# Optimization experiments

Hardware: AMD Instinct MI355X
Metric: run time of the kernel (lower is better)

The kernel has to match this reference:

```python
import jax, jax.numpy as jnp
import numpy as np

N = 100000
E = 1600000
NFEAT = 128
NHID = 16
HEADS = 4
NCLASS = 40
NEG_SLOPE = 0.2
BN_EPS = 1e-5


def setup_inputs() -> dict:
    key = jax.random.key(0)
    ks = jax.random.split(key, 16)
    HC = NHID * HEADS  # 64
    x = jax.random.normal(ks[0], (N, NFEAT), dtype=jnp.float32)
    edge_index = jax.random.randint(ks[1], (2, E), 0, N, dtype=jnp.int64)
    def glorot(k, shape, fan_in):
        return jax.random.normal(k, shape, dtype=jnp.float32) * (1.0 / np.sqrt(fan_in))
    return {
        "x": x,
        "edge_index": edge_index,
        # layer 1: GATConv(NFEAT -> NHID, heads=HEADS, concat=True)
        "W1": glorot(ks[2], (NFEAT, HC), NFEAT),
        "att_src1": glorot(ks[3], (HEADS, NHID), NHID),
        "att_dst1": glorot(ks[4], (HEADS, NHID), NHID),
        "bias1": jnp.zeros((HC,), dtype=jnp.float32),
        # BatchNorm1d(HC), eval mode (running stats)
        "bn_gamma": jnp.ones((HC,), dtype=jnp.float32),
        "bn_beta": jnp.zeros((HC,), dtype=jnp.float32),
        "bn_mean": jax.random.normal(ks[5], (HC,), dtype=jnp.float32) * 0.1,
        "bn_var": jax.random.uniform(ks[6], (HC,), dtype=jnp.float32, minval=0.5, maxval=1.5),
        # layer 2: GATConv(HC -> NCLASS, heads=1, concat=False)
        "W2": glorot(ks[7], (HC, NCLASS), HC),
        "att_src2": glorot(ks[8], (1, NCLASS), NCLASS),
        "att_dst2": glorot(ks[9], (1, NCLASS), NCLASS),
        "bias2": jnp.zeros((NCLASS,), dtype=jnp.float32),
    }


def gat_conv(x, src, dst, W, att_src, att_dst, bias, concat):
    """PyG GATConv (eval; self-loops assumed already appended to src/dst)."""
    H, C = att_src.shape
    n = x.shape[0]
    h = (x @ W).reshape(n, H, C)                         # [N,H,C]
    a_s = (h * att_src[None]).sum(-1)                    # [N,H]
    a_d = (h * att_dst[None]).sum(-1)                    # [N,H]
    alpha = jax.nn.leaky_relu(a_s[src] + a_d[dst], NEG_SLOPE)  # [Et,H]
    # segment softmax over incoming edges of each destination node
    amax = jax.ops.segment_max(alpha, dst, num_segments=n)    # [N,H]
    ex = jnp.exp(alpha - amax[dst])
    denom = jax.ops.segment_sum(ex, dst, num_segments=n)
    coef = ex / denom[dst]                               # [Et,H]
    msg = h[src] * coef[:, :, None]                      # [Et,H,C]
    out = jax.ops.segment_sum(msg, dst, num_segments=n)  # [N,H,C]
    out = out.reshape(n, H * C) if concat else out.mean(axis=1)
    return out + bias


def reference(x, edge_index, W1, att_src1, att_dst1, bias1,
              bn_gamma, bn_beta, bn_mean, bn_var,
              W2, att_src2, att_dst2, bias2):
    n = x.shape[0]
    loops = jnp.arange(n, dtype=edge_index.dtype)
    src = jnp.concatenate([edge_index[0], loops])
    dst = jnp.concatenate([edge_index[1], loops])
    h = gat_conv(x, src, dst, W1, att_src1, att_dst1, bias1, concat=True)
    h = (h - bn_mean) * jax.lax.rsqrt(bn_var + BN_EPS) * bn_gamma + bn_beta
    h = jax.nn.relu(h)  # dropout is identity in eval
    out = gat_conv(h, src, dst, W2, att_src2, att_dst2, bias2, concat=False)
    return out
```

## Files before the change

kernel.cpp:

```cpp
#include <hip/hip_runtime.h>
#include <hip/hip_bf16.h>
#include <hip/hip_fp16.h>

#define NFEAT  128
#define HC     64
#define HEADS  4
#define NHID   16
#define NCLASS 40
#define NEG    0.2f
#define BN_EPS 1e-5f

#define BK_SH   9
#define CHUNK   8192
#define STAGE   12288

typedef _Float16 half8_t __attribute__((ext_vector_type(8)));
typedef float    f32x4_t __attribute__((ext_vector_type(4)));

__device__ __forceinline__ float leaky(float a) { return (a > 0.f) ? a : NEG * a; }

__global__ __launch_bounds__(256) void k_gemm1(
    const float* __restrict__ x, const float* __restrict__ W1,
    const float* __restrict__ att_s, const float* __restrict__ att_d,
    __half* __restrict__ h1, float* __restrict__ as1, float* __restrict__ ad1,
    int n)
{
    const int wave = threadIdx.x >> 6, lane = threadIdx.x & 63;
    const int quad = lane >> 4, l16 = lane & 15;

    half8_t bfrag[4][4];
    #pragma unroll
    for (int ks = 0; ks < 4; ++ks)
        #pragma unroll
        for (int ct = 0; ct < 4; ++ct)
            #pragma unroll
            for (int j = 0; j < 8; ++j)
                bfrag[ks][ct][j] =
                    (_Float16)W1[(ks * 32 + quad * 8 + j) * HC + ct * 16 + l16];

    float avs[4], avd[4];
    #pragma unroll
    for (int ct = 0; ct < 4; ++ct) {
        avs[ct] = att_s[ct * 16 + l16];
        avd[ct] = att_d[ct * 16 + l16];
    }

    const int nslab = (n + 15) >> 4;
    for (int slab = blockIdx.x * 4 + wave; slab < nslab; slab += gridDim.x * 4) {
        const int rowbase = slab * 16;
        const int arow = min(rowbase + l16, n - 1);
        const float* xp = x + (size_t)arow * NFEAT;

        f32x4_t acc[4] = {{0.f,0.f,0.f,0.f},{0.f,0.f,0.f,0.f},
                          {0.f,0.f,0.f,0.f},{0.f,0.f,0.f,0.f}};
        #pragma unroll
        for (int ks = 0; ks < 4; ++ks) {
            const float4 xa = *(const float4*)(xp + ks * 32 + quad * 8);
            const float4 xb = *(const float4*)(xp + ks * 32 + quad * 8 + 4);
            half8_t af;
            af[0] = (_Float16)xa.x; af[1] = (_Float16)xa.y;
            af[2] = (_Float16)xa.z; af[3] = (_Float16)xa.w;
            af[4] = (_Float16)xb.x; af[5] = (_Float16)xb.y;
            af[6] = (_Float16)xb.z; af[7] = (_Float16)xb.w;
            #pragma unroll
            for (int ct = 0; ct < 4; ++ct)
                acc[ct] = __builtin_amdgcn_mfma_f32_16x16x32_f16(
                    af, bfrag[ks][ct], acc[ct], 0, 0, 0);
        }

        #pragma unroll
        for (int reg = 0; reg < 4; ++reg) {
            const int row = rowbase + quad * 4 + reg;
            const bool valid = row < n;

            float4 ps, pd;
            ps.x = acc[0][reg] * avs[0]; pd.x = acc[0][reg] * avd[0];
            ps.y = acc[1][reg] * avs[1]; pd.y = acc[1][reg] * avd[1];
            ps.z = acc[2][reg] * avs[2]; pd.z = acc[2][reg] * avd[2];
            ps.w = acc[3][reg] * avs[3]; pd.w = acc[3][reg] * avd[3];
            #pragma unroll
            for (int off = 8; off >= 1; off >>= 1) {
                ps.x += __shfl_xor(ps.x, off, 64); pd.x += __shfl_xor(pd.x, off, 64);
                ps.y += __shfl_xor(ps.y, off, 64); pd.y += __shfl_xor(pd.y, off, 64);
                ps.z += __shfl_xor(ps.z, off, 64); pd.z += __shfl_xor(pd.z, off, 64);
                ps.w += __shfl_xor(ps.w, off, 64); pd.w += __shfl_xor(pd.w, off, 64);
            }
            if (valid) {
                #pragma unroll
                for (int ct = 0; ct < 4; ++ct)
                    h1[(size_t)row * HC + ct * 16 + l16] =
                        __float2half_rn(acc[ct][reg]);
                if (l16 == 0) {
                    *(float4*)(as1 + (size_t)row * HEADS) = ps;
                    *(float4*)(ad1 + (size_t)row * HEADS) = pd;
                }
            }
        }
    }
}

__global__ __launch_bounds__(256) void k_hist(
    const int* __restrict__ edst, int* __restrict__ hist, int E, int nbk)
{
    __shared__ int lh[256];
    const int w = blockIdx.x, t = threadIdx.x;
    for (int i = t; i < nbk; i += 256) lh[i] = 0;
    __syncthreads();
    const int lo = w * CHUNK, hi = min(E, lo + CHUNK);
    for (int e = lo + t; e < hi; e += 256)
        atomicAdd(&lh[edst[e] >> BK_SH], 1);
    __syncthreads();
    for (int i = t; i < nbk; i += 256) hist[(size_t)w * nbk + i] = lh[i];
}

__global__ __launch_bounds__(256) void k_colscan(
    int* __restrict__ hist, int* __restrict__ colsum, int nbk, int nw)
{
    __shared__ int wred[4];
    const int b = blockIdx.x, t = threadIdx.x;
    const int lane = t & 63, w = t >> 6;
    const int v = (t < nw) ? hist[(size_t)t * nbk + b] : 0;
    int sc = v;
    #pragma unroll
    for (int off = 1; off < 64; off <<= 1) {
        int u = __shfl_up(sc, off, 64);
        if (lane >= off) sc += u;
    }
    if (lane == 63) wred[w] = sc;
    __syncthreads();
    if (t == 0) { int a = 0; for (int i = 0; i < 4; ++i) { int xx = wred[i]; wred[i] = a; a += xx; } }
    __syncthreads();
    const int excl = sc - v + wred[w];
    if (t < nw) hist[(size_t)t * nbk + b] = excl;
    if (t == nw - 1) colsum[b] = excl + v;
}

__global__ __launch_bounds__(256) void k_bscan(
    const int* __restrict__ colsum, int* __restrict__ bstart, int nbk, int E)
{
    __shared__ int wred[4];
    const int t = threadIdx.x, lane = t & 63, w = t >> 6;
    const int v = (t < nbk) ? colsum[t] : 0;
    int sc = v;
    #pragma unroll
    for (int off = 1; off < 64; off <<= 1) {
        int u = __shfl_up(sc, off, 64);
        if (lane >= off) sc += u;
    }
    if (lane == 63) wred[w] = sc;
    __syncthreads();
    if (t == 0) { int a = 0; for (int i = 0; i < 4; ++i) { int xx = wred[i]; wred[i] = a; a += xx; } }
    __syncthreads();
    if (t < nbk) bstart[t] = sc - v + wred[w];
    if (t == 0) bstart[nbk] = E;
}

__global__ __launch_bounds__(256) void k_scatter(
    const int* __restrict__ esrc, const int* __restrict__ edst,
    const int* __restrict__ hist, const int* __restrict__ bstart,
    int2* __restrict__ pairs, int E, int nbk)
{
    __shared__ int cur[256];
    const int w = blockIdx.x, t = threadIdx.x;
    for (int i = t; i < nbk; i += 256)
        cur[i] = bstart[i] + hist[(size_t)w * nbk + i];
    __syncthreads();
    const int lo = w * CHUNK, hi = min(E, lo + CHUNK);
    for (int e = lo + t; e < hi; e += 256) {
        const int s = esrc[e], d = edst[e];
        const int pos = atomicAdd(&cur[d >> BK_SH], 1);
        pairs[pos] = make_int2(s, d);
    }
}

__global__ __launch_bounds__(256) void k_build(
    const int2* __restrict__ pairs, const int* __restrict__ bstart,
    int* __restrict__ rowptr, int* __restrict__ csr, int n, int nbk)
{
    __shared__ int cnt[512];
    __shared__ int cur[512];
    __shared__ int stage[STAGE];
    __shared__ int wred[4];
    const int b = blockIdx.x, t = threadIdx.x;
    const int base = bstart[b], eend = bstart[b + 1], m = eend - base;
    const int n0 = b << BK_SH;
    const int nn = min(512, n - n0);

    cnt[t] = 0; cnt[t + 256] = 0;
    __syncthreads();
    for (int e = base + t; e < eend; e += 256)
        atomicAdd(&cnt[pairs[e].y - n0], 1);
    __syncthreads();

    const int c0 = cnt[2 * t], c1 = cnt[2 * t + 1];
    const int s = c0 + c1;
    const int lane = t & 63, w = t >> 6;
    int sc = s;
    #pragma unroll
    for (int off = 1; off < 64; off <<= 1) {
        int u = __shfl_up(sc, off, 64);
        if (lane >= off) sc += u;
    }
    if (lane == 63) wred[w] = sc;
    __syncthreads();
    if (t == 0) { int a = 0; for (int i = 0; i < 4; ++i) { int xx = wred[i]; wred[i] = a; a += xx; } }
    __syncthreads();
    const int excl = sc - s + wred[w];
    cur[2 * t]     = excl;
    cur[2 * t + 1] = excl + c0;
    if (2 * t < nn)     rowptr[n0 + 2 * t]     = base + excl + c0;
    if (2 * t + 1 < nn) rowptr[n0 + 2 * t + 1] = base + excl + c0 + c1;
    __syncthreads();

    for (int e = base + t; e < eend; e += 256) {
        const int2 p = pairs[e];
        const int loc = atomicAdd(&cur[p.y - n0], 1);
        if (loc < STAGE) stage[loc] = p.x;
        else             csr[base + loc] = p.x;
    }
    __syncthreads();
    const int lim = min(m, STAGE);
    for (int i = t; i < lim; i += 256) csr[base + i] = stage[i];
}

__global__ __launch_bounds__(256) void k_agg1(
    const int* __restrict__ csr, const int* __restrict__ rowptr,
    const __half* __restrict__ h1, const float* __restrict__ as1,
    const float* __restrict__ ad1,
    const float* __restrict__ bias1, const float* __restrict__ gamma,
    const float* __restrict__ beta, const float* __restrict__ mean,
    const float* __restrict__ var,
    const float* __restrict__ W2, const float* __restrict__ ats2,
    const float* __restrict__ atd2,
    __half* __restrict__ g, float* __restrict__ as2o, float* __restrict__ ad2o,
    int n)
{
    __shared__ float sW[NCLASS * HC];
    __shared__ float sh[16][68];
    __shared__ float sE[16][132];
    __shared__ int   sS[16][33];
    for (int i = threadIdx.x; i < NCLASS * HC; i += 256) sW[i] = W2[i];
    __syncthreads();

    const int gi = threadIdx.x >> 4;
    const int q  = threadIdx.x & 15;
    const int myh = q >> 2;

    const float4 b1v = *(const float4*)(bias1 + 4 * q);
    const float4 gmv = *(const float4*)(gamma + 4 * q);
    const float4 vrv = *(const float4*)(var   + 4 * q);
    const float4 mnv = *(const float4*)(mean  + 4 * q);
    const float4 btv = *(const float4*)(beta  + 4 * q);
    float4 scv, shv;
    scv.x = gmv.x * rsqrtf(vrv.x + BN_EPS);
    scv.y = gmv.y * rsqrtf(vrv.y + BN_EPS);
    scv.z = gmv.z * rsqrtf(vrv.z + BN_EPS);
    scv.w = gmv.w * rsqrtf(vrv.w + BN_EPS);
    shv.x = btv.x - mnv.x * scv.x;
    shv.y = btv.y - mnv.y * scv.y;
    shv.z = btv.z - mnv.z * scv.z;
    shv.w = btv.w - mnv.w * scv.w;
    float4 at2 = {0.f, 0.f, 0.f, 0.f}, dt2 = {0.f, 0.f, 0.f, 0.f};
    if (q < 10) {
        at2 = *(const float4*)(ats2 + 4 * q);
        dt2 = *(const float4*)(atd2 + 4 * q);
    }

    for (int node0 = blockIdx.x * 16; node0 < n; node0 += gridDim.x * 16) {
        const int node = node0 + gi;
        if (node >= n) continue;

        const float4 adv = *(const float4*)(ad1 + node * HEADS);
        const float4 sv4 = *(const float4*)(as1 + node * HEADS);
        float4 eself;
        eself.x = __expf(leaky(sv4.x + adv.x));
        eself.y = __expf(leaky(sv4.y + adv.y));
        eself.z = __expf(leaky(sv4.z + adv.z));
        eself.w = __expf(leaky(sv4.w + adv.w));
        const float es = (myh == 0) ? eself.x : (myh == 1) ? eself.y
                       : (myh == 2) ? eself.z : eself.w;

        float2 raws = *(const float2*)(h1 + (size_t)node * HC + 4 * q);
        const float2 s0 = __half22float2(*(__half2*)&raws.x);
        const float2 s1 = __half22float2(*(__half2*)&raws.y);
        float4 acc;
        acc.x = es * s0.x; acc.y = es * s0.y;
        acc.z = es * s1.x; acc.w = es * s1.y;
        float4 dpart = {0.f, 0.f, 0.f, 0.f};

        const int start = (node == 0) ? 0 : rowptr[node - 1];
        const int end   = rowptr[node];

        for (int base = start; base < end; base += 32) {
            const int m = min(32, end - base);
            float4 ea = {0.f, 0.f, 0.f, 0.f}, eb = {0.f, 0.f, 0.f, 0.f};
            int ia = 0, ib = 0;
            if (q < m) {
                ia = csr[base + q];
                const float4 s4 = *(const float4*)(as1 + (size_t)ia * HEADS);
                ea.x = __expf(leaky(s4.x + adv.x));
                ea.y = __expf(leaky(s4.y + adv.y));
                ea.z = __expf(leaky(s4.z + adv.z));
                ea.w = __expf(leaky(s4.w + adv.w));
            }
            if (q + 16 < m) {
                ib = csr[base + q + 16];
                const float4 s4 = *(const float4*)(as1 + (size_t)ib * HEADS);
                eb.x = __expf(leaky(s4.x + adv.x));
                eb.y = __expf(leaky(s4.y + adv.y));
                eb.z = __expf(leaky(s4.z + adv.z));
                eb.w = __expf(leaky(s4.w + adv.w));
            }
            dpart.x += ea.x + eb.x; dpart.y += ea.y + eb.y;
            dpart.z += ea.z + eb.z; dpart.w += ea.w + eb.w;
            *(float4*)&sE[gi][4 * q] = ea;
            *(float4*)&sE[gi][4 * (q + 16)] = eb;
            sS[gi][q] = ia; sS[gi][q + 16] = ib;
            __threadfence_block();

            int j = 0;
            for (; j + 2 <= m; j += 2) {
                const int sa = sS[gi][j], sb = sS[gi][j + 1];
                const float fa = sE[gi][4 * j + myh];
                const float fb = sE[gi][4 * (j + 1) + myh];
                const float2 ra = *(const float2*)(h1 + (size_t)sa * HC + 4 * q);
                const float2 rb = *(const float2*)(h1 + (size_t)sb * HC + 4 * q);
                const float2 a0 = __half22float2(*(const __half2*)&ra.x);
                const float2 a1 = __half22float2(*(const __half2*)&ra.y);
                const float2 b0 = __half22float2(*(const __half2*)&rb.x);
                const float2 b1 = __half22float2(*(const __half2*)&rb.y);
                acc.x = fmaf(fa, a0.x, acc.x); acc.y = fmaf(fa, a0.y, acc.y);
                acc.z = fmaf(fa, a1.x, acc.z); acc.w = fmaf(fa, a1.y, acc.w);
                acc.x = fmaf(fb, b0.x, acc.x); acc.y = fmaf(fb, b0.y, acc.y);
                acc.z = fmaf(fb, b1.x, acc.z); acc.w = fmaf(fb, b1.y, acc.w);
            }
            if (j < m) {
                const int sa = sS[gi][j];
                const float fa = sE[gi][4 * j + myh];
                const float2 ra = *(const float2*)(h1 + (size_t)sa * HC + 4 * q);
                const float2 a0 = __half22float2(*(const __half2*)&ra.x);
                const float2 a1 = __half22float2(*(const __half2*)&ra.y);
                acc.x = fmaf(fa, a0.x, acc.x); acc.y = fmaf(fa, a0.y, acc.y);
                acc.z = fmaf(fa, a1.x, acc.z); acc.w = fmaf(fa, a1.y, acc.w);
            }
            __threadfence_block();
        }

        #pragma unroll
        for (int off = 8; off >= 1; off >>= 1) {
            dpart.x += __shfl_xor(dpart.x, off, 64);
            dpart.y += __shfl_xor(dpart.y, off, 64);
            dpart.z += __shfl_xor(dpart.z, off, 64);
            dpart.w += __shfl_xor(dpart.w, off, 64);
        }
        const float den = es + ((myh == 0) ? dpart.x : (myh == 1) ? dpart.y
                               : (myh == 2) ? dpart.z : dpart.w);
        const float rden = 1.f / den;

        float4 v;
        v.x = fmaxf(fmaf(acc.x * rden + b1v.x, scv.x, shv.x), 0.f);
        v.y = fmaxf(fmaf(acc.y * rden + b1v.y, scv.y, shv.y), 0.f);
        v.z = fmaxf(fmaf(acc.z * rden + b1v.z, scv.z, shv.z), 0.f);
        v.w = fmaxf(fmaf(acc.w * rden + b1v.w, scv.w, shv.w), 0.f);
        *(float4*)&sh[gi][4 * q] = v;
        __threadfence_block();

        float4 gacc = {0.f, 0.f, 0.f, 0.f};
        if (q < 10) {
            #pragma unroll 8
            for (int k = 0; k < HC; ++k) {
                const float hk = sh[gi][k];
                const float4 wv = *(const float4*)&sW[k * NCLASS + 4 * q];
                gacc.x = fmaf(hk, wv.x, gacc.x);
                gacc.y = fmaf(hk, wv.y, gacc.y);
                gacc.z = fmaf(hk, wv.z, gacc.z);
                gacc.w = fmaf(hk, wv.w, gacc.w);
            }
        }
        __half2 p0 = __float22half2_rn({gacc.x, gacc.y});
        __half2 p1 = __float22half2_rn({gacc.z, gacc.w});
        float2 packed; *(__half2*)&packed.x = p0; *(__half2*)&packed.y = p1;
        *(float2*)(g + (size_t)node * HC + 4 * q) = packed;

        float sv = gacc.x * at2.x + gacc.y * at2.y + gacc.z * at2.z + gacc.w * at2.w;
        float dv = gacc.x * dt2.x + gacc.y * dt2.y + gacc.z * dt2.z + gacc.w * dt2.w;
        #pragma unroll
        for (int off = 8; off >= 1; off >>= 1) {
            sv += __shfl_xor(sv, off, 64);
            dv += __shfl_xor(dv, off, 64);
        }
        if (q == 0) { as2o[node] = sv; ad2o[node] = dv; }
        __threadfence_block();
    }
}

__global__ __launch_bounds__(256) void k_agg2(
    const int* __restrict__ csr, const int* __restrict__ rowptr,
    const __half* __restrict__ g, const float* __restrict__ as2,
    const float* __restrict__ ad2, const float* __restrict__ bias2,
    float* __restrict__ out, int n)
{
    __shared__ float sE[16][34];
    __shared__ int   sS[16][33];
    const int gi = threadIdx.x >> 4;
    const int q  = threadIdx.x & 15;

    float4 b2v = {0.f, 0.f, 0.f, 0.f};
    if (q < 10) b2v = *(const float4*)(bias2 + 4 * q);

    for (int node0 = blockIdx.x * 16; node0 < n; node0 += gridDim.x * 16) {
        const int node = node0 + gi;
        if (node >= n) continue;

        const float ad2d = ad2[node];
        const float eself = __expf(leaky(as2[node] + ad2d));

        float2 raws = *(const float2*)(g + (size_t)node * HC + 4 * q);
        const float2 s0 = __half22float2(*(__half2*)&raws.x);
        const float2 s1 = __half22float2(*(__half2*)&raws.y);
        float4 acc;
        acc.x = eself * s0.x; acc.y = eself * s0.y;
        acc.z = eself * s1.x; acc.w = eself * s1.y;
        float dpart = 0.f;

        const int start = (node == 0) ? 0 : rowptr[node - 1];
        const int end   = rowptr[node];

        for (int base = start; base < end; base += 32) {
            const int m = min(32, end - base);
            float ea = 0.f, eb = 0.f;
            int ia = 0, ib = 0;
            if (q < m) {
                ia = csr[base + q];
                ea = __expf(leaky(as2[ia] + ad2d));
            }
            if (q + 16 < m) {
                ib = csr[base + q + 16];
                eb = __expf(leaky(as2[ib] + ad2d));
            }
            dpart += ea + eb;
            sE[gi][q] = ea; sE[gi][q + 16] = eb;
            sS[gi][q] = ia; sS[gi][q + 16] = ib;
            __threadfence_block();

            int j = 0;
            for (; j + 2 <= m; j += 2) {
                const int sa = sS[gi][j], sb = sS[gi][j + 1];
                const float fa = sE[gi][j], fb = sE[gi][j + 1];
                const float2 ra = *(const float2*)(g + (size_t)sa * HC + 4 * q);
                const float2 rb = *(const float2*)(g + (size_t)sb * HC + 4 * q);
                const float2 a0 = __half22float2(*(const __half2*)&ra.x);
                const float2 a1 = __half22float2(*(const __half2*)&ra.y);
                const float2 b0 = __half22float2(*(const __half2*)&rb.x);
                const float2 b1 = __half22float2(*(const __half2*)&rb.y);
                acc.x = fmaf(fa, a0.x, acc.x); acc.y = fmaf(fa, a0.y, acc.y);
                acc.z = fmaf(fa, a1.x, acc.z); acc.w = fmaf(fa, a1.y, acc.w);
                acc.x = fmaf(fb, b0.x, acc.x); acc.y = fmaf(fb, b0.y, acc.y);
                acc.z = fmaf(fb, b1.x, acc.z); acc.w = fmaf(fb, b1.y, acc.w);
            }
            if (j < m) {
                const int sa = sS[gi][j];
                const float fa = sE[gi][j];
                const float2 ra = *(const float2*)(g + (size_t)sa * HC + 4 * q);
                const float2 a0 = __half22float2(*(const __half2*)&ra.x);
                const float2 a1 = __half22float2(*(const __half2*)&ra.y);
                acc.x = fmaf(fa, a0.x, acc.x); acc.y = fmaf(fa, a0.y, acc.y);
                acc.z = fmaf(fa, a1.x, acc.z); acc.w = fmaf(fa, a1.y, acc.w);
            }
            __threadfence_block();
        }

        #pragma unroll
        for (int off = 8; off >= 1; off >>= 1)
            dpart += __shfl_xor(dpart, off, 64);
        const float rden = 1.f / (dpart + eself);

        if (q < 10) {
            float4 r;
            r.x = acc.x * rden + b2v.x;
            r.y = acc.y * rden + b2v.y;
            r.z = acc.z * rden + b2v.z;
            r.w = acc.w * rden + b2v.w;
            *(float4*)(out + (size_t)node * NCLASS + 4 * q) = r;
        }
    }
}

extern "C" void kernel_launch(void* const* d_in, const int* in_sizes, int n_in,
                              void* d_out, int out_size, void* d_ws, size_t ws_size,
                              hipStream_t stream)
{
    const float* x    = (const float*)d_in[0];
    const int*   ei   = (const int*)  d_in[1];
    const float* W1   = (const float*)d_in[2];
    const float* as1w = (const float*)d_in[3];
    const float* ad1w = (const float*)d_in[4];
    const float* b1   = (const float*)d_in[5];
    const float* gm   = (const float*)d_in[6];
    const float* bt   = (const float*)d_in[7];
    const float* mn   = (const float*)d_in[8];
    const float* vr   = (const float*)d_in[9];
    const float* W2   = (const float*)d_in[10];
    const float* as2w = (const float*)d_in[11];
    const float* ad2w = (const float*)d_in[12];
    const float* b2   = (const float*)d_in[13];

    const int n = in_sizes[0] / NFEAT;
    const int E = in_sizes[1] / 2;
    const int* esrc = ei;
    const int* edst = ei + E;

    const int nbk = (n + 511) >> BK_SH;
    const int nw  = (E + CHUNK - 1) / CHUNK;

    float*  ws   = (float*)d_ws;
    __half* h1   = (__half*)ws;
    float*  a_s1 = ws   + (size_t)n * 32;
    float*  a_d1 = a_s1 + (size_t)n * 4;
    __half* gbuf = (__half*)(a_d1 + (size_t)n * 4);
    float*  a_s2 = a_d1 + (size_t)n * 4 + (size_t)n * 32;
    float*  a_d2 = a_s2 + n;
    int2*   pairs  = (int2*)(a_d2 + n);
    int*    csr    = (int*)(pairs + E);
    int*    rowptr = csr + E;
    int*    hist   = rowptr + n;
    int*    colsum = hist + (size_t)nw * nbk;
    int*    bstart = colsum + nbk;
    float*  outv = (float*)d_out;

    const int nblk = (n + 15) / 16;

    k_hist   <<<nw, 256, 0, stream>>>(edst, hist, E, nbk);
    k_colscan<<<nbk, 256, 0, stream>>>(hist, colsum, nbk, nw);
    k_bscan  <<<1, 256, 0, stream>>>(colsum, bstart, nbk, E);
    k_scatter<<<nw, 256, 0, stream>>>(esrc, edst, hist, bstart, pairs, E, nbk);
    k_build  <<<nbk, 256, 0, stream>>>(pairs, bstart, rowptr, csr, n, nbk);
    k_gemm1  <<<512, 256, 0, stream>>>(x, W1, as1w, ad1w, h1, a_s1, a_d1, n);
    k_agg1   <<<nblk, 256, 0, stream>>>(csr, rowptr, h1, a_s1, a_d1, b1, gm, bt, mn, vr,
                                        W2, as2w, ad2w, gbuf, a_s2, a_d2, n);
    k_agg2   <<<nblk, 256, 0, stream>>>(csr, rowptr, gbuf, a_s2, a_d2, b2, outv, n);
}
```

Measured before the change: 295.4 us.

## Sort nodes by in-degree for balanced aggregation, prefetch gathers, fp16 W2 in LDS

Adds a degree histogram, a scan and a fill pass that build a permutation grouping nodes of similar in-degree. Both aggregation kernels then process nodes in that order, so the 16-thread groups within a wave have similar loop trip counts and less divergence. The neighbor gather loops are software-pipelined so the next pair of rows is loaded before the current pair is used. W2 is stored as fp16 in shared memory to halve its LDS footprint. The costs are three extra small kernels plus a memset, scattered node accesses through perm, and slightly lower precision in the second-layer projection.

Result: slower. 594.1 us (+101.1%).

```diff
diff --git a/kernel.cpp b/kernel.cpp
--- a/kernel.cpp
+++ b/kernel.cpp
@@ -15,6 +15,7 @@
 #define STAGE   12288
 
 typedef _Float16 half8_t __attribute__((ext_vector_type(8)));
+typedef _Float16 half4_t __attribute__((ext_vector_type(4)));
 typedef float    f32x4_t __attribute__((ext_vector_type(4)));
 
 __device__ __forceinline__ float leaky(float a) { return (a > 0.f) ? a : NEG * a; }
@@ -223,8 +224,52 @@
     for (int i = t; i < lim; i += 256) csr[base + i] = stage[i];
 }
 
+__global__ __launch_bounds__(256) void k_dhist(
+    const int* __restrict__ rowptr, int* __restrict__ dhist, int n)
+{
+    __shared__ int lh[128];
+    if (threadIdx.x < 128) lh[threadIdx.x] = 0;
+    __syncthreads();
+    for (int i = blockIdx.x * 256 + threadIdx.x; i < n; i += gridDim.x * 256) {
+        const int d = min(rowptr[i] - (i ? rowptr[i - 1] : 0), 127);
+        atomicAdd(&lh[d], 1);
+    }
+    __syncthreads();
+    if (threadIdx.x < 128 && lh[threadIdx.x])
+        atomicAdd(&dhist[threadIdx.x], lh[threadIdx.x]);
+}
+
+__global__ __launch_bounds__(128) void k_dscan(
+    const int* __restrict__ dhist, int* __restrict__ dcur)
+{
+    __shared__ int ws2[2];
+    const int t = threadIdx.x, lane = t & 63, w = t >> 6;
+    const int v = dhist[t];
+    int sc = v;
+    #pragma unroll
+    for (int off = 1; off < 64; off <<= 1) {
+        int u = __shfl_up(sc, off, 64);
+        if (lane >= off) sc += u;
+    }
+    if (lane == 63) ws2[w] = sc;
+    __syncthreads();
+    dcur[t] = sc - v + ((w == 1) ? ws2[0] : 0);
+}
+
+__global__ __launch_bounds__(256) void k_dfill(
+    const int* __restrict__ rowptr, int* __restrict__ dcur,
+    int* __restrict__ perm, int n)
+{
+    for (int i = blockIdx.x * 256 + threadIdx.x; i < n; i += gridDim.x * 256) {
+        const int d = min(rowptr[i] - (i ? rowptr[i - 1] : 0), 127);
+        const int pos = atomicAdd(&dcur[d], 1);
+        perm[pos] = i;
+    }
+}
+
 __global__ __launch_bounds__(256) void k_agg1(
     const int* __restrict__ csr, const int* __restrict__ rowptr,
+    const int* __restrict__ perm,
     const __half* __restrict__ h1, const float* __restrict__ as1,
     const float* __restrict__ ad1,
     const float* __restrict__ bias1, const float* __restrict__ gamma,
@@ -235,11 +280,11 @@
     __half* __restrict__ g, float* __restrict__ as2o, float* __restrict__ ad2o,
     int n)
 {
-    __shared__ float sW[NCLASS * HC];
+    __shared__ _Float16 sWh[NCLASS * HC];
     __shared__ float sh[16][68];
     __shared__ float sE[16][132];
     __shared__ int   sS[16][33];
-    for (int i = threadIdx.x; i < NCLASS * HC; i += 256) sW[i] = W2[i];
+    for (int i = threadIdx.x; i < NCLASS * HC; i += 256) sWh[i] = (_Float16)W2[i];
     __syncthreads();
 
     const int gi = threadIdx.x >> 4;
@@ -267,8 +312,9 @@
     }
 
     for (int node0 = blockIdx.x * 16; node0 < n; node0 += gridDim.x * 16) {
-        const int node = node0 + gi;
-        if (node >= n) continue;
+        const int idx = node0 + gi;
+        if (idx >= n) continue;
+        const int node = perm[idx];
 
         const float4 adv = *(const float4*)(ad1 + node * HEADS);
         const float4 sv4 = *(const float4*)(as1 + node * HEADS);
@@ -281,11 +327,11 @@
                        : (myh == 2) ? eself.z : eself.w;
 
         float2 raws = *(const float2*)(h1 + (size_t)node * HC + 4 * q);
-        const float2 s0 = __half22float2(*(__half2*)&raws.x);
-        const float2 s1 = __half22float2(*(__half2*)&raws.y);
+        const float2 s0v = __half22float2(*(__half2*)&raws.x);
+        const float2 s1v = __half22float2(*(__half2*)&raws.y);
         float4 acc;
-        acc.x = es * s0.x; acc.y = es * s0.y;
-        acc.z = es * s1.x; acc.w = es * s1.y;
+        acc.x = es * s0v.x; acc.y = es * s0v.y;
+        acc.z = es * s1v.x; acc.w = es * s1v.y;
         float4 dpart = {0.f, 0.f, 0.f, 0.f};
 
         const int start = (node == 0) ? 0 : rowptr[node - 1];
@@ -318,30 +364,41 @@
             sS[gi][q] = ia; sS[gi][q + 16] = ib;
             __threadfence_block();
 
+            const int*   sB = &sS[gi][0];
+            const float* eB = &sE[gi][0];
             int j = 0;
-            for (; j + 2 <= m; j += 2) {
-                const int sa = sS[gi][j], sb = sS[gi][j + 1];
-                const float fa = sE[gi][4 * j + myh];
-                const float fb = sE[gi][4 * (j + 1) + myh];
-                const float2 ra = *(const float2*)(h1 + (size_t)sa * HC + 4 * q);
-                const float2 rb = *(const float2*)(h1 + (size_t)sb * HC + 4 * q);
-                const float2 a0 = __half22float2(*(const __half2*)&ra.x);
-                const float2 a1 = __half22float2(*(const __half2*)&ra.y);
-                const float2 b0 = __half22float2(*(const __half2*)&rb.x);
-                const float2 b1 = __half22float2(*(const __half2*)&rb.y);
-                acc.x = fmaf(fa, a0.x, acc.x); acc.y = fmaf(fa, a0.y, acc.y);
-                acc.z = fmaf(fa, a1.x, acc.z); acc.w = fmaf(fa, a1.y, acc.w);
-                acc.x = fmaf(fb, b0.x, acc.x); acc.y = fmaf(fb, b0.y, acc.y);
-                acc.z = fmaf(fb, b1.x, acc.z); acc.w = fmaf(fb, b1.y, acc.w);
-            }
-            if (j < m) {
-                const int sa = sS[gi][j];
-                const float fa = sE[gi][4 * j + myh];
-                const float2 ra = *(const float2*)(h1 + (size_t)sa * HC + 4 * q);
-                const float2 a0 = __half22float2(*(const __half2*)&ra.x);
-                const float2 a1 = __half22float2(*(const __half2*)&ra.y);
-                acc.x = fmaf(fa, a0.x, acc.x); acc.y = fmaf(fa, a0.y, acc.y);
-                acc.z = fmaf(fa, a1.x, acc.z); acc.w = fmaf(fa, a1.y, acc.w);
+            const int sa0 = sB[0];
+            const int sa1 = sB[(m > 1) ? 1 : 0];
+            float2 w0 = *(const float2*)(h1 + (size_t)sa0 * HC + 4 * q);
+            float2 w1 = *(const float2*)(h1 + (size_t)sa1 * HC + 4 * q);
+            for (; j + 2 < m; j += 2) {
+                const int sn0 = sB[j + 2];
+                const int sn1 = sB[(j + 3 < m) ? (j + 3) : (j + 2)];
+                const float2 v0 = *(const float2*)(h1 + (size_t)sn0 * HC + 4 * q);
+                const float2 v1 = *(const float2*)(h1 + (size_t)sn1 * HC + 4 * q);
+                const float e0 = eB[(j + 0) * 4 + myh];
+                const float e1 = eB[(j + 1) * 4 + myh];
+                const float2 a0 = __half22float2(*(const __half2*)&w0.x);
+                const float2 a1 = __half22float2(*(const __half2*)&w0.y);
+                const float2 b0 = __half22float2(*(const __half2*)&w1.x);
+                const float2 b1 = __half22float2(*(const __half2*)&w1.y);
+                acc.x = fmaf(e0, a0.x, acc.x); acc.y = fmaf(e0, a0.y, acc.y);
+                acc.z = fmaf(e0, a1.x, acc.z); acc.w = fmaf(e0, a1.y, acc.w);
+                acc.x = fmaf(e1, b0.x, acc.x); acc.y = fmaf(e1, b0.y, acc.y);
+                acc.z = fmaf(e1, b1.x, acc.z); acc.w = fmaf(e1, b1.y, acc.w);
+                w0 = v0; w1 = v1;
+            }
+            {
+                const float e0 = eB[j * 4 + myh];
+                const float e1 = (j + 1 < m) ? eB[(j + 1) * 4 + myh] : 0.f;
+                const float2 a0 = __half22float2(*(const __half2*)&w0.x);
+                const float2 a1 = __half22float2(*(const __half2*)&w0.y);
+                const float2 b0 = __half22float2(*(const __half2*)&w1.x);
+                const float2 b1 = __half22float2(*(const __half2*)&w1.y);
+                acc.x = fmaf(e0, a0.x, acc.x); acc.y = fmaf(e0, a0.y, acc.y);
+                acc.z = fmaf(e0, a1.x, acc.z); acc.w = fmaf(e0, a1.y, acc.w);
+                acc.x = fmaf(e1, b0.x, acc.x); acc.y = fmaf(e1, b0.y, acc.y);
+                acc.z = fmaf(e1, b1.x, acc.z); acc.w = fmaf(e1, b1.y, acc.w);
             }
             __threadfence_block();
         }
@@ -370,11 +427,11 @@
             #pragma unroll 8
             for (int k = 0; k < HC; ++k) {
                 const float hk = sh[gi][k];
-                const float4 wv = *(const float4*)&sW[k * NCLASS + 4 * q];
-                gacc.x = fmaf(hk, wv.x, gacc.x);
-                gacc.y = fmaf(hk, wv.y, gacc.y);
-                gacc.z = fmaf(hk, wv.z, gacc.z);
-                gacc.w = fmaf(hk, wv.w, gacc.w);
+                const half4_t wv = *(const half4_t*)&sWh[k * NCLASS + 4 * q];
+                gacc.x = fmaf(hk, (float)wv[0], gacc.x);
+                gacc.y = fmaf(hk, (float)wv[1], gacc.y);
+                gacc.z = fmaf(hk, (float)wv[2], gacc.z);
+                gacc.w = fmaf(hk, (float)wv[3], gacc.w);
             }
         }
         __half2 p0 = __float22half2_rn({gacc.x, gacc.y});
@@ -396,6 +453,7 @@
 
 __global__ __launch_bounds__(256) void k_agg2(
     const int* __restrict__ csr, const int* __restrict__ rowptr,
+    const int* __restrict__ perm,
     const __half* __restrict__ g, const float* __restrict__ as2,
     const float* __restrict__ ad2, const float* __restrict__ bias2,
     float* __restrict__ out, int n)
@@ -409,18 +467,19 @@
     if (q < 10) b2v = *(const float4*)(bias2 + 4 * q);
 
     for (int node0 = blockIdx.x * 16; node0 < n; node0 += gridDim.x * 16) {
-        const int node = node0 + gi;
-        if (node >= n) continue;
+        const int idx = node0 + gi;
+        if (idx >= n) continue;
+        const int node = perm[idx];
 
         const float ad2d = ad2[node];
         const float eself = __expf(leaky(as2[node] + ad2d));
 
         float2 raws = *(const float2*)(g + (size_t)node * HC + 4 * q);
-        const float2 s0 = __half22float2(*(__half2*)&raws.x);
-        const float2 s1 = __half22float2(*(__half2*)&raws.y);
+        const float2 s0v = __half22float2(*(__half2*)&raws.x);
+        const float2 s1v = __half22float2(*(__half2*)&raws.y);
         float4 acc;
-        acc.x = eself * s0.x; acc.y = eself * s0.y;
-        acc.z = eself * s1.x; acc.w = eself * s1.y;
+        acc.x = eself * s0v.x; acc.y = eself * s0v.y;
+        acc.z = eself * s1v.x; acc.w = eself * s1v.y;
         float dpart = 0.f;
 
         const int start = (node == 0) ? 0 : rowptr[node - 1];
@@ -443,29 +502,41 @@
             sS[gi][q] = ia; sS[gi][q + 16] = ib;
             __threadfence_block();
 
+            const int*   sB = &sS[gi][0];
+            const float* eB = &sE[gi][0];
             int j = 0;
-            for (; j + 2 <= m; j += 2) {
-                const int sa = sS[gi][j], sb = sS[gi][j + 1];
-                const float fa = sE[gi][j], fb = sE[gi][j + 1];
-                const float2 ra = *(const float2*)(g + (size_t)sa * HC + 4 * q);
-                const float2 rb = *(const float2*)(g + (size_t)sb * HC + 4 * q);
-                const float2 a0 = __half22float2(*(const __half2*)&ra.x);
-                const float2 a1 = __half22float2(*(const __half2*)&ra.y);
-                const float2 b0 = __half22float2(*(const __half2*)&rb.x);
-                const float2 b1 = __half22float2(*(const __half2*)&rb.y);
-                acc.x = fmaf(fa, a0.x, acc.x); acc.y = fmaf(fa, a0.y, acc.y);
-                acc.z = fmaf(fa, a1.x, acc.z); acc.w = fmaf(fa, a1.y, acc.w);
-                acc.x = fmaf(fb, b0.x, acc.x); acc.y = fmaf(fb, b0.y, acc.y);
-                acc.z = fmaf(fb, b1.x, acc.z); acc.w = fmaf(fb, b1.y, acc.w);
-            }
-            if (j < m) {
-                const int sa = sS[gi][j];
-                const float fa = sE[gi][j];
-                const float2 ra = *(const float2*)(g + (size_t)sa * HC + 4 * q);
-                const float2 a0 = __half22float2(*(const __half2*)&ra.x);
-                const float2 a1 = __half22float2(*(const __half2*)&ra.y);
-                acc.x = fmaf(fa, a0.x, acc.x); acc.y = fmaf(fa, a0.y, acc.y);
-                acc.z = fmaf(fa, a1.x, acc.z); acc.w = fmaf(fa, a1.y, acc.w);
+            const int sa0 = sB[0];
+            const int sa1 = sB[(m > 1) ? 1 : 0];
+            float2 w0 = *(const float2*)(g + (size_t)sa0 * HC + 4 * q);
+            float2 w1 = *(const float2*)(g + (size_t)sa1 * HC + 4 * q);
+            for (; j + 2 < m; j += 2) {
+                const int sn0 = sB[j + 2];
+                const int sn1 = sB[(j + 3 < m) ? (j + 3) : (j + 2)];
+                const float2 v0 = *(const float2*)(g + (size_t)sn0 * HC + 4 * q);
+                const float2 v1 = *(const float2*)(g + (size_t)sn1 * HC + 4 * q);
+                const float e0 = eB[j + 0];
+                const float e1 = eB[j + 1];
+                const float2 a0 = __half22float2(*(const __half2*)&w0.x);
+                const float2 a1 = __half22float2(*(const __half2*)&w0.y);
+                const float2 b0 = __half22float2(*(const __half2*)&w1.x);
+                const float2 b1 = __half22float2(*(const __half2*)&w1.y);
+                acc.x = fmaf(e0, a0.x, acc.x); acc.y = fmaf(e0, a0.y, acc.y);
+                acc.z = fmaf(e0, a1.x, acc.z); acc.w = fmaf(e0, a1.y, acc.w);
+                acc.x = fmaf(e1, b0.x, acc.x); acc.y = fmaf(e1, b0.y, acc.y);
+                acc.z = fmaf(e1, b1.x, acc.z); acc.w = fmaf(e1, b1.y, acc.w);
+                w0 = v0; w1 = v1;
+            }
+            {
+                const float e0 = eB[j];
+                const float e1 = (j + 1 < m) ? eB[j + 1] : 0.f;
+                const float2 a0 = __half22float2(*(const __half2*)&w0.x);
+                const float2 a1 = __half22float2(*(const __half2*)&w0.y);
+                const float2 b0 = __half22float2(*(const __half2*)&w1.x);
+                const float2 b1 = __half22float2(*(const __half2*)&w1.y);
+                acc.x = fmaf(e0, a0.x, acc.x); acc.y = fmaf(e0, a0.y, acc.y);
+                acc.z = fmaf(e0, a1.x, acc.z); acc.w = fmaf(e0, a1.y, acc.w);
+                acc.x = fmaf(e1, b0.x, acc.x); acc.y = fmaf(e1, b0.y, acc.y);
+                acc.z = fmaf(e1, b1.x, acc.z); acc.w = fmaf(e1, b1.y, acc.w);
             }
             __threadfence_block();
         }
@@ -526,17 +597,27 @@
     int*    hist   = rowptr + n;
     int*    colsum = hist + (size_t)nw * nbk;
     int*    bstart = colsum + nbk;
+    int*    perm   = bstart + (nbk + 1);
+    int*    dhist  = perm + n;
+    int*    dcur   = dhist + 128;
     float*  outv = (float*)d_out;
 
     const int nblk = (n + 15) / 16;
+
+    hipMemsetAsync(dhist, 0, 256 * sizeof(int), stream);
 
     k_hist   <<<nw, 256, 0, stream>>>(edst, hist, E, nbk);
     k_colscan<<<nbk, 256, 0, stream>>>(hist, colsum, nbk, nw);
     k_bscan  <<<1, 256, 0, stream>>>(colsum, bstart, nbk, E);
     k_scatter<<<nw, 256, 0, stream>>>(esrc, edst, hist, bstart, pairs, E, nbk);
     k_build  <<<nbk, 256, 0, stream>>>(pairs, bstart, rowptr, csr, n, nbk);
+    k_dhist  <<<256, 256, 0, stream>>>(rowptr, dhist, n);
+    k_dscan  <<<1, 128, 0, stream>>>(dhist, dcur);
+    k_dfill  <<<256, 256, 0, stream>>>(rowptr, dcur, perm, n);
     k_gemm1  <<<512, 256, 0, stream>>>(x, W1, as1w, ad1w, h1, a_s1, a_d1, n);
-    k_agg1   <<<nblk, 256, 0, stream>>>(csr, rowptr, h1, a_s1, a_d1, b1, gm, bt, mn, vr,
+    k_agg1   <<<nblk, 256, 0, stream>>>(csr, rowptr, perm, h1, a_s1, a_d1,
+                                        b1, gm, bt, mn, vr,
                                         W2, as2w, ad2w, gbuf, a_s2, a_d2, n);
-    k_agg2   <<<nblk, 256, 0, stream>>>(csr, rowptr, gbuf, a_s2, a_d2, b2, outv, n);
-}
+    k_agg2   <<<nblk, 256, 0, stream>>>(csr, rowptr, perm, gbuf, a_s2, a_d2,
+                                        b2, outv, n);
+}
```
